# Optimization experiments

Measured on AMD Instinct MI355X. Metric: run time of the kernel, lower is better.

Reference implementation:

```python
import jax, jax.numpy as jnp
import numpy as np
import math

BATCH, TBINS, SPATIAL = 16, 8, 16
WIN, SHIFT = 8, 4
DIM, HEADS = 1024, 16
HD = DIM // HEADS
N = WIN * WIN          # tokens per window = 64
NW = (SPATIAL // WIN) ** 2  # windows per image = 4
HIDDEN = 4 * DIM


def _static_buffers():
    ws = WIN
    # continuous relative coords table (signed log-spaced), [(2ws-1)^2, 2]
    c = np.arange(-(ws - 1), ws, dtype=np.float32) / (ws - 1)
    c = np.sign(c) * np.log2(1.0 + np.abs(c))
    gh, gw = np.meshgrid(c, c, indexing='ij')
    table = np.stack([gh, gw], axis=-1).reshape(-1, 2).astype(np.float32)
    # relative position index, [N, N]
    coords = np.stack(np.meshgrid(np.arange(ws), np.arange(ws), indexing='ij')).reshape(2, -1)
    rel = (coords[:, :, None] - coords[:, None, :]).transpose(1, 2, 0)
    rel[..., 0] += ws - 1
    rel[..., 1] += ws - 1
    rel[..., 0] *= 2 * ws - 1
    rp_idx = rel.sum(-1)  # [N, N] int
    # shifted-window attention mask, [NW, N, N]
    img = np.zeros((SPATIAL, SPATIAL), dtype=np.float32)
    slices = [slice(0, -ws), slice(-ws, -SHIFT), slice(-SHIFT, None)]
    cnt = 0
    for hs in slices:
        for wsl in slices:
            img[hs, wsl] = cnt
            cnt += 1
    mw = img.reshape(SPATIAL // ws, ws, SPATIAL // ws, ws).transpose(0, 2, 1, 3).reshape(-1, ws * ws)
    diff = mw[:, None, :] - mw[:, :, None]  # matches unsqueeze(1) - unsqueeze(2)
    attn_mask = np.where(diff != 0, np.float32(-100.0), np.float32(0.0))
    return jnp.asarray(table), jnp.asarray(rp_idx), jnp.asarray(attn_mask)

CPB_TABLE, RP_IDX, ATTN_MASK = _static_buffers()


def _window_partition(x):  # [B, H, W, C] -> [B*nW, ws, ws, C]
    b, h, w, c = x.shape
    x = x.reshape(b, h // WIN, WIN, w // WIN, WIN, c).transpose(0, 1, 3, 2, 4, 5)
    return x.reshape(-1, WIN, WIN, c)


def _window_reverse(win, h, w):  # [B*nW, ws, ws, C] -> [B, H, W, C]
    b = win.shape[0] // ((h // WIN) * (w // WIN))
    x = win.reshape(b, h // WIN, w // WIN, WIN, WIN, -1).transpose(0, 1, 3, 2, 4, 5)
    return x.reshape(b, h, w, -1)


def _layernorm(x, g, b):
    m = jnp.mean(x, -1, keepdims=True)
    v = jnp.mean((x - m) ** 2, -1, keepdims=True)
    return (x - m) * jax.lax.rsqrt(v + 1e-5) * g + b


def _l2norm(x):
    return x / jnp.maximum(jnp.linalg.norm(x, axis=-1, keepdims=True), 1e-12)


def setup_inputs() -> dict:
    key = jax.random.key(0)
    ks = jax.random.split(key, 16)
    s = 0.02
    inp = {
        'x': jax.random.normal(ks[0], (BATCH, TBINS * SPATIAL * SPATIAL, DIM), jnp.float32),
        'qkv_w': jax.random.normal(ks[1], (3 * DIM, DIM), jnp.float32) * s,
        'q_bias': jnp.zeros((DIM,), jnp.float32),
        'v_bias': jnp.zeros((DIM,), jnp.float32),
        'logit_scale': jnp.full((HEADS, 1, 1), math.log(10.0), jnp.float32),
        'cpb_w1': jax.random.normal(ks[2], (512, 2), jnp.float32) * s,
        'cpb_b1': jnp.zeros((512,), jnp.float32),
        'cpb_w2': jax.random.normal(ks[3], (HEADS, 512), jnp.float32) * s,
        'proj_w': jax.random.normal(ks[4], (DIM, DIM), jnp.float32) * s,
        'proj_b': jnp.zeros((DIM,), jnp.float32),
        'norm1_w': jnp.ones((DIM,), jnp.float32),
        'norm1_b': jnp.zeros((DIM,), jnp.float32),
        'fc1_w': jax.random.normal(ks[5], (HIDDEN, DIM), jnp.float32) * s,
        'fc1_b': jnp.zeros((HIDDEN,), jnp.float32),
        'fc2_w': jax.random.normal(ks[6], (DIM, HIDDEN), jnp.float32) * s,
        'fc2_b': jnp.zeros((DIM,), jnp.float32),
        'norm2_w': jnp.ones((DIM,), jnp.float32),
        'norm2_b': jnp.zeros((DIM,), jnp.float32),
    }
    return inp


def reference(x, qkv_w, q_bias, v_bias, logit_scale, cpb_w1, cpb_b1, cpb_w2,
              proj_w, proj_b, norm1_w, norm1_b, fc1_w, fc1_b, fc2_w, fc2_b,
              norm2_w, norm2_b):
    B, L, C = x.shape
    xs = x.reshape(B * TBINS, SPATIAL, SPATIAL, C)
    shortcut = xs
    # cyclic shift
    shifted = jnp.roll(xs, shift=(-SHIFT, -SHIFT), axis=(1, 2))
    xw = _window_partition(shifted).reshape(-1, N, C)  # [Bw, N, C]
    Bw = xw.shape[0]

    # qkv with q/v bias only (no k bias)
    qkv_bias = jnp.concatenate([q_bias, jnp.zeros_like(v_bias), v_bias])
    qkv = xw @ qkv_w.T + qkv_bias
    qkv = qkv.reshape(Bw, N, 3, HEADS, HD).transpose(2, 0, 3, 1, 4)
    q, k, v = qkv[0], qkv[1], qkv[2]  # [Bw, h, N, hd]

    # cosine attention with clamped learnable logit scale
    attn = jnp.einsum('bhnd,bhmd->bhnm', _l2norm(q), _l2norm(k))
    scale = jnp.exp(jnp.minimum(logit_scale, math.log(100.0)))  # [h,1,1]
    attn = attn * scale[None]

    # continuous relative position bias via CPB-MLP
    tbl = jax.nn.relu(CPB_TABLE @ cpb_w1.T + cpb_b1) @ cpb_w2.T  # [(2ws-1)^2, h]
    tbl = 16.0 * jax.nn.sigmoid(tbl)
    bias = tbl[RP_IDX.reshape(-1)].reshape(N, N, HEADS).transpose(2, 0, 1)  # [h,N,N]
    attn = attn + bias[None]

    # shift mask
    attn = attn.reshape(Bw // NW, NW, HEADS, N, N) + ATTN_MASK[None, :, None]
    attn = attn.reshape(Bw, HEADS, N, N)
    attn = jax.nn.softmax(attn, axis=-1)

    out = jnp.einsum('bhnm,bhmd->bhnd', attn, v)
    out = out.transpose(0, 2, 1, 3).reshape(Bw, N, C)
    out = out @ proj_w.T + proj_b

    out = _window_reverse(out.reshape(-1, WIN, WIN, C), SPATIAL, SPATIAL)
    out = jnp.roll(out, shift=(SHIFT, SHIFT), axis=(1, 2))

    # SwinV2 post-norm residuals
    xs = shortcut + _layernorm(out, norm1_w, norm1_b)
    h = jax.nn.gelu(xs @ fc1_w.T + fc1_b, approximate=False) @ fc2_w.T + fc2_b
    xs = xs + _layernorm(h, norm2_w, norm2_b)
    return xs.reshape(B, L, C)
```

## Files before the change

kernel.cpp:

```cpp
#include <hip/hip_runtime.h>
#include <hip/hip_bf16.h>
#include <math.h>

typedef __hip_bfloat16 bf16;
typedef __attribute__((ext_vector_type(8))) short short8;
typedef __attribute__((ext_vector_type(4))) short short4v;
typedef __attribute__((ext_vector_type(4))) float floatx4;
typedef __attribute__((ext_vector_type(2))) unsigned int uint2v;

#define DEV static __device__ __forceinline__

DEV float bf2f(unsigned short u) {
  union { unsigned int i; float f; } x;
  x.i = ((unsigned int)u) << 16;
  return x.f;
}
DEV unsigned short f2bf_bits(float f) {
  union { bf16 h; unsigned short u; } x;
  x.h = __float2bfloat16(f);
  return x.u;
}
DEV short8 cvt8(float4 a, float4 b) {
  short8 r;
  r[0] = (short)f2bf_bits(a.x); r[1] = (short)f2bf_bits(a.y);
  r[2] = (short)f2bf_bits(a.z); r[3] = (short)f2bf_bits(a.w);
  r[4] = (short)f2bf_bits(b.x); r[5] = (short)f2bf_bits(b.y);
  r[6] = (short)f2bf_bits(b.z); r[7] = (short)f2bf_bits(b.w);
  return r;
}

DEV float gelu_fast(float v) {
  float y = v * (1.5957691216f + 0.0713548163f * v * v);
  return __fdividef(v, 1.f + __expf(-y));
}

DEV void gload_lds16(const unsigned short* g, unsigned short* l) {
  __builtin_amdgcn_global_load_lds((const __attribute__((address_space(1))) void*)g,
                                   (__attribute__((address_space(3))) void*)l,
                                   16, 0, 0);
}

DEV unsigned lds_addr(const void* p) {
  return (unsigned)(unsigned long long)(const __attribute__((address_space(3))) char*)p;
}

DEV int gather_win_row(int wr) {
  int bw = wr >> 6, n = wr & 63;
  int bt = bw >> 2, w2 = bw & 3;
  int wi = w2 >> 1, wj = w2 & 1;
  int r = n >> 3, c = n & 7;
  int sr = (wi * 8 + r + 4) & 15;
  int sc = (wj * 8 + c + 4) & 15;
  return bt * 256 + sr * 16 + sc;
}

enum { BIAS_SIMPLE = 0, BIAS_QKV = 1 };
enum { ACT_NONE = 0, ACT_GELU = 1 };

__global__ __launch_bounds__(256) void cvt_bf16(const float* __restrict__ in,
                                                bf16* __restrict__ out, int n) {
  int i = (blockIdx.x * 256 + threadIdx.x) * 8;
  if (i >= n) return;
  float4 a = *reinterpret_cast<const float4*>(in + i);
  float4 b = *reinterpret_cast<const float4*>(in + i + 4);
  *reinterpret_cast<short8*>((unsigned short*)out + i) = cvt8(a, b);
}

#define VMCNT(N_) asm volatile("s_waitcnt vmcnt(" #N_ ")" ::: "memory")
#define WAITLGKM() do { asm volatile("s_waitcnt lgkmcnt(0)" ::: "memory"); \
                        __builtin_amdgcn_sched_barrier(0); } while (0)
#define BARRIER() __builtin_amdgcn_s_barrier()
#define DSR(dst, addr, OFF) \
  asm volatile("ds_read_b128 %0, %1 offset:" #OFF : "=v"(dst) : "v"(addr) : "memory")

#define STG8(BUF, ISB, KS, KT) do { \
    unsigned short* d_ = (unsigned short*)(smem + (BUF) * 65536 + (ISB) * 32768 + (KS) * 16384); \
    gload_lds16(((ISB) ? bgp[0] : agp[0]) + (KT) * 64 + (KS) * 32, d_ + tid * 8); \
    gload_lds16(((ISB) ? bgp[1] : agp[1]) + (KT) * 64 + (KS) * 32, d_ + 4096 + tid * 8); \
  } while (0)

#define RD_A8(CUR, KS, IH) do { \
    unsigned a_ = smemBase + (CUR) * 65536 + (KS) * 16384 + aB0 + (IH) * 4096; \
    DSR(af[0], a_, 0); DSR(af[1], a_, 1024); DSR(af[2], a_, 2048); DSR(af[3], a_, 3072); \
  } while (0)

#define RD_B8(CUR, KS) do { \
    unsigned b_ = smemBase + (CUR) * 65536 + 32768 + (KS) * 16384 + bB0; \
    DSR(bfr[0], b_, 0); DSR(bfr[1], b_, 1024); DSR(bfr[2], b_, 2048); DSR(bfr[3], b_, 3072); \
  } while (0)

#define MFMA16(IH) do { \
    __builtin_amdgcn_s_setprio(1); \
    _Pragma("unroll") \
    for (int i_ = 0; i_ < 4; ++i_) \
      _Pragma("unroll") \
      for (int j_ = 0; j_ < 4; ++j_) \
        acc[(IH) * 4 + i_][j_] = __builtin_amdgcn_mfma_f32_16x16x32_bf16( \
            af[i_], bfr[j_], acc[(IH) * 4 + i_][j_], 0, 0, 0); \
    __builtin_amdgcn_s_setprio(0); \
  } while (0)

template <int GATHER, int BIASMODE, int ACT>
__global__ __launch_bounds__(512, 2) void gemm8p(
    const unsigned short* __restrict__ A, const unsigned short* __restrict__ B,
    const float* __restrict__ bias0, const float* __restrict__ bias1,
    bf16* __restrict__ C, int M, int N, int K)
{
  extern __shared__ __align__(16) char smem[];
  const int tid = threadIdx.x;
  const int lane = tid & 63;
  const int wave = tid >> 6;
  const int wm = wave >> 2, wn = wave & 3;
  const int l15 = lane & 15, g = lane >> 4;
  const int xr = (l15 >> 1) & 3;

  const int gy = gridDim.y;
  const int nwg = gridDim.x * gy;
  int lin = blockIdx.y * gridDim.x + blockIdx.x;
  if ((nwg & 7) == 0) lin = (lin & 7) * (nwg >> 3) + (lin >> 3);
  const int tileM = (lin / gy) * 256;
  const int tileN = (lin % gy) * 256;

  const unsigned short* agp[2];
  const unsigned short* bgp[2];
#pragma unroll
  for (int u = 0; u < 2; ++u) {
    int s = u * 512 + tid;
    int row = s >> 2;
    int dslot = (s & 3) ^ ((s >> 3) & 3);
    int gr = tileM + row;
    int sr = GATHER ? gather_win_row(gr) : gr;
    agp[u] = A + (size_t)sr * (size_t)K + dslot * 8;
    bgp[u] = B + (size_t)(tileN + row) * (size_t)K + dslot * 8;
  }

  const unsigned smemBase = lds_addr(smem);
  const unsigned aB0 = (unsigned)((wm * 128 + l15) * 64 + ((g ^ xr) * 16));
  const unsigned bB0 = (unsigned)((wn * 64 + l15) * 64 + ((g ^ xr) * 16));

  floatx4 acc[8][4];
#pragma unroll
  for (int i = 0; i < 8; ++i)
#pragma unroll
    for (int j = 0; j < 4; ++j) acc[i][j] = (floatx4){0.f, 0.f, 0.f, 0.f};

  short8 af[4], bfr[4];
  const int NT = K >> 6;
  int cur = 0;

  STG8(0, 0, 0, 0); STG8(0, 1, 0, 0); STG8(0, 0, 1, 0); STG8(0, 1, 1, 0);
  VMCNT(0);
  BARRIER();

  for (int t = 0; t < NT - 1; ++t) {
    const int nb = cur ^ 1;
    RD_B8(cur, 0); RD_A8(cur, 0, 0);
    STG8(nb, 0, 0, t + 1);
    BARRIER(); WAITLGKM(); MFMA16(0); BARRIER();
    RD_A8(cur, 0, 1);
    STG8(nb, 1, 0, t + 1);
    VMCNT(4);
    BARRIER(); WAITLGKM(); MFMA16(1); BARRIER();
    RD_B8(cur, 1); RD_A8(cur, 1, 0);
    STG8(nb, 0, 1, t + 1);
    BARRIER(); WAITLGKM(); MFMA16(0); BARRIER();
    RD_A8(cur, 1, 1);
    STG8(nb, 1, 1, t + 1);
    VMCNT(4);
    BARRIER(); WAITLGKM(); MFMA16(1); BARRIER();
    cur = nb;
  }
  RD_B8(cur, 0); RD_A8(cur, 0, 0);
  BARRIER(); WAITLGKM(); MFMA16(0); BARRIER();
  RD_A8(cur, 0, 1);
  VMCNT(0);
  BARRIER(); WAITLGKM(); MFMA16(1); BARRIER();
  RD_B8(cur, 1); RD_A8(cur, 1, 0);
  BARRIER(); WAITLGKM(); MFMA16(0); BARRIER();
  RD_A8(cur, 1, 1);
  WAITLGKM(); MFMA16(1);

  __syncthreads();
  unsigned short* sh16 = (unsigned short*)smem;
  const int q = l15;
  float bv[4];
#pragma unroll
  for (int j = 0; j < 4; ++j) {
    const int colG = tileN + wn * 64 + j * 16 + q;
    if (BIASMODE == BIAS_QKV) {
      bv[j] = (colG < 1024) ? bias0[colG] : (colG < 2048 ? 0.f : bias1[colG - 2048]);
    } else {
      bv[j] = bias0[colG];
    }
  }
#pragma unroll
  for (int h = 0; h < 2; ++h) {
    if (wm == h) {
#pragma unroll
      for (int i = 0; i < 8; ++i)
#pragma unroll
        for (int j = 0; j < 4; ++j)
#pragma unroll
          for (int r = 0; r < 4; ++r) {
            float v = acc[i][j][r] + bv[j];
            if (ACT == ACT_GELU) v = gelu_fast(v);
            sh16[(i * 16 + g * 4 + r) * 264 + wn * 64 + j * 16 + q] = f2bf_bits(v);
          }
    }
    __syncthreads();
#pragma unroll
    for (int pass = 0; pass < 8; ++pass) {
      const int idx = pass * 512 + tid;
      const int row = idx >> 5, c16 = idx & 31;
      uint4 val = *reinterpret_cast<const uint4*>(&sh16[row * 264 + c16 * 8]);
      *reinterpret_cast<uint4*>(
          (unsigned short*)C + (size_t)(tileM + h * 128 + row) * (size_t)N +
          tileN + c16 * 8) = val;
    }
    __syncthreads();
  }
}

#define STG_A2(BUF, KS, KT) do { \
    unsigned short* d_ = (unsigned short*)(smem + (BUF) * 49152 + (KS) * 16384); \
    gload_lds16(agp[0] + (KT) * 64 + (KS) * 32, d_ + tid * 8); \
    gload_lds16(agp[1] + (KT) * 64 + (KS) * 32, d_ + 4096 + tid * 8); \
  } while (0)

#define STG_B1(BUF, KS, KT) do { \
    unsigned short* d_ = (unsigned short*)(smem + (BUF) * 49152 + 32768 + (KS) * 8192); \
    gload_lds16(bgp0 + (KT) * 64 + (KS) * 32, d_ + tid * 8); \
  } while (0)

#define RD_A8N(CUR, KS, IH) do { \
    unsigned a_ = smemBase + (CUR) * 49152 + (KS) * 16384 + aB0 + (IH) * 4096; \
    DSR(af[0], a_, 0); DSR(af[1], a_, 1024); DSR(af[2], a_, 2048); DSR(af[3], a_, 3072); \
  } while (0)

#define RD_B2N(CUR, KS) do { \
    unsigned b_ = smemBase + (CUR) * 49152 + 32768 + (KS) * 8192 + bB0; \
    DSR(bfr[0], b_, 0); DSR(bfr[1], b_, 1024); \
  } while (0)

#define MFMA8(IH) do { \
    __builtin_amdgcn_s_setprio(1); \
    _Pragma("unroll") \
    for (int i_ = 0; i_ < 4; ++i_) \
      _Pragma("unroll") \
      for (int j_ = 0; j_ < 2; ++j_) \
        acc[(IH) * 4 + i_][j_] = __builtin_amdgcn_mfma_f32_16x16x32_bf16( \
            af[i_], bfr[j_], acc[(IH) * 4 + i_][j_], 0, 0, 0); \
    __builtin_amdgcn_s_setprio(0); \
  } while (0)

template <int GATHER, int BIASMODE, int ACT>
__global__ __launch_bounds__(512, 2) void gemm8pn(
    const unsigned short* __restrict__ A, const unsigned short* __restrict__ B,
    const float* __restrict__ bias0, const float* __restrict__ bias1,
    bf16* __restrict__ C, int M, int N, int K)
{
  extern __shared__ __align__(16) char smem[];
  const int tid = threadIdx.x;
  const int lane = tid & 63;
  const int wave = tid >> 6;
  const int wm = wave >> 2, wn = wave & 3;
  const int l15 = lane & 15, g = lane >> 4;
  const int xr = (l15 >> 1) & 3;

  const int gy = gridDim.y;
  const int nwg = gridDim.x * gy;
  int lin = blockIdx.y * gridDim.x + blockIdx.x;
  if ((nwg & 7) == 0) lin = (lin & 7) * (nwg >> 3) + (lin >> 3);
  const int tileM = (lin / gy) * 256;
  const int tileN = (lin % gy) * 128;

  const unsigned short* agp[2];
#pragma unroll
  for (int u = 0; u < 2; ++u) {
    int s = u * 512 + tid;
    int row = s >> 2;
    int dslot = (s & 3) ^ ((s >> 3) & 3);
    int gr = tileM + row;
    int sr = GATHER ? gather_win_row(gr) : gr;
    agp[u] = A + (size_t)sr * (size_t)K + dslot * 8;
  }
  const unsigned short* bgp0 =
      B + (size_t)(tileN + (tid >> 2)) * (size_t)K + ((tid & 3) ^ ((tid >> 3) & 3)) * 8;

  const unsigned smemBase = lds_addr(smem);
  const unsigned aB0 = (unsigned)((wm * 128 + l15) * 64 + ((g ^ xr) * 16));
  const unsigned bB0 = (unsigned)((wn * 32 + l15) * 64 + ((g ^ xr) * 16));

  floatx4 acc[8][2];
#pragma unroll
  for (int i = 0; i < 8; ++i)
#pragma unroll
    for (int j = 0; j < 2; ++j) acc[i][j] = (floatx4){0.f, 0.f, 0.f, 0.f};

  short8 af[4], bfr[2];
  const int NT = K >> 6;
  int cur = 0;

  STG_A2(0, 0, 0); STG_B1(0, 0, 0); STG_A2(0, 1, 0); STG_B1(0, 1, 0);
  VMCNT(0);
  BARRIER();

  for (int t = 0; t < NT - 1; ++t) {
    const int nb = cur ^ 1;
    RD_B2N(cur, 0); RD_A8N(cur, 0, 0);
    STG_A2(nb, 0, t + 1);
    BARRIER(); WAITLGKM(); MFMA8(0); BARRIER();
    RD_A8N(cur, 0, 1);
    STG_B1(nb, 0, t + 1);
    VMCNT(3);
    BARRIER(); WAITLGKM(); MFMA8(1); BARRIER();
    RD_B2N(cur, 1); RD_A8N(cur, 1, 0);
    STG_A2(nb, 1, t + 1);
    BARRIER(); WAITLGKM(); MFMA8(0); BARRIER();
    RD_A8N(cur, 1, 1);
    STG_B1(nb, 1, t + 1);
    VMCNT(3);
    BARRIER(); WAITLGKM(); MFMA8(1); BARRIER();
    cur = nb;
  }
  RD_B2N(cur, 0); RD_A8N(cur, 0, 0);
  BARRIER(); WAITLGKM(); MFMA8(0); BARRIER();
  RD_A8N(cur, 0, 1);
  VMCNT(0);
  BARRIER(); WAITLGKM(); MFMA8(1); BARRIER();
  RD_B2N(cur, 1); RD_A8N(cur, 1, 0);
  BARRIER(); WAITLGKM(); MFMA8(0); BARRIER();
  RD_A8N(cur, 1, 1);
  WAITLGKM(); MFMA8(1);

  __syncthreads();
  unsigned short* sh16 = (unsigned short*)smem;
  const int q = l15;
  float bv[2];
#pragma unroll
  for (int j = 0; j < 2; ++j) {
    const int colG = tileN + wn * 32 + j * 16 + q;
    if (BIASMODE == BIAS_QKV) {
      bv[j] = (colG < 1024) ? bias0[colG] : (colG < 2048 ? 0.f : bias1[colG - 2048]);
    } else {
      bv[j] = bias0[colG];
    }
  }
#pragma unroll
  for (int h = 0; h < 2; ++h) {
    if (wm == h) {
#pragma unroll
      for (int i = 0; i < 8; ++i)
#pragma unroll
        for (int j = 0; j < 2; ++j)
#pragma unroll
          for (int r = 0; r < 4; ++r) {
            float v = acc[i][j][r] + bv[j];
            if (ACT == ACT_GELU) v = gelu_fast(v);
            sh16[(i * 16 + g * 4 + r) * 136 + wn * 32 + j * 16 + q] = f2bf_bits(v);
          }
    }
    __syncthreads();
#pragma unroll
    for (int pass = 0; pass < 4; ++pass) {
      const int idx = pass * 512 + tid;
      const int row = idx >> 4, c16 = idx & 15;
      uint4 val = *reinterpret_cast<const uint4*>(&sh16[row * 136 + c16 * 8]);
      *reinterpret_cast<uint4*>(
          (unsigned short*)C + (size_t)(tileM + h * 128 + row) * (size_t)N +
          tileN + c16 * 8) = val;
    }
    __syncthreads();
  }
}

template <int GATHER, int BIASMODE, int ACT>
__global__ __launch_bounds__(256, 2) void gemm_bt(
    const unsigned short* __restrict__ A, const unsigned short* __restrict__ B,
    const float* __restrict__ bias0, const float* __restrict__ bias1,
    bf16* __restrict__ C, int M, int N, int K)
{
  __shared__ __align__(16) unsigned short sh[128 * 136];
  unsigned short* As = sh;
  unsigned short* Bs = sh + 8192;

  const int tid = threadIdx.x;
  const int lane = tid & 63;
  const int wave = tid >> 6;
  const int waveM = wave >> 1, waveN = wave & 1;
  const int tileM = blockIdx.x * 128, tileN = blockIdx.y * 128;

  const int row0 = tid >> 3;
  const int kOff = (tid & 7) * 8;

  const unsigned short* ag[4];
  const unsigned short* bg[4];
  unsigned short* al[4];
  unsigned short* bl[4];
#pragma unroll
  for (int t = 0; t < 4; ++t) {
    int gr = tileM + row0 + 32 * t;
    int sr = GATHER ? gather_win_row(gr) : gr;
    ag[t] = A + (size_t)sr * (size_t)K + (size_t)kOff;
    bg[t] = B + (size_t)(tileN + row0 + 32 * t) * (size_t)K + (size_t)kOff;
    al[t] = &As[(row0 + 32 * t) * 64 + kOff];
    bl[t] = &Bs[(row0 + 32 * t) * 64 + kOff];
  }

  floatx4 acc[4][4];
#pragma unroll
  for (int i = 0; i < 4; ++i)
#pragma unroll
    for (int j = 0; j < 4; ++j) acc[i][j] = (floatx4){0.f, 0.f, 0.f, 0.f};

  for (int k0 = 0; k0 < K; k0 += 64) {
#pragma unroll
    for (int t = 0; t < 4; ++t) {
      gload_lds16(ag[t] + k0, al[t]);
      gload_lds16(bg[t] + k0, bl[t]);
    }
    __syncthreads();
#pragma unroll
    for (int ks = 0; ks < 2; ++ks) {
      const int kk = ks * 32 + (lane >> 4) * 8;
      short8 afv[4], bfv[4];
#pragma unroll
      for (int i = 0; i < 4; ++i)
        afv[i] = *reinterpret_cast<const short8*>(
            &As[(waveM * 64 + i * 16 + (lane & 15)) * 64 + kk]);
#pragma unroll
      for (int j = 0; j < 4; ++j)
        bfv[j] = *reinterpret_cast<const short8*>(
            &Bs[(waveN * 64 + j * 16 + (lane & 15)) * 64 + kk]);
#pragma unroll
      for (int i = 0; i < 4; ++i)
#pragma unroll
        for (int j = 0; j < 4; ++j)
          acc[i][j] = __builtin_amdgcn_mfma_f32_16x16x32_bf16(afv[i], bfv[j], acc[i][j], 0, 0, 0);
    }
    __syncthreads();
  }

#pragma unroll
  for (int j = 0; j < 4; ++j) {
    const int colL = waveN * 64 + j * 16 + (lane & 15);
    const int colG = tileN + colL;
    float bv;
    if (BIASMODE == BIAS_QKV) {
      if (colG < 1024) bv = bias0[colG];
      else if (colG < 2048) bv = 0.f;
      else bv = bias1[colG - 2048];
    } else {
      bv = bias0[colG];
    }
#pragma unroll
    for (int i = 0; i < 4; ++i) {
      const int rL = waveM * 64 + i * 16 + ((lane >> 4) * 4);
#pragma unroll
      for (int r = 0; r < 4; ++r) {
        float v = acc[i][j][r] + bv;
        if (ACT == ACT_GELU) v = gelu_fast(v);
        sh[(rL + r) * 136 + colL] = f2bf_bits(v);
      }
    }
  }
  __syncthreads();
  {
    const int rowR = tid >> 4;
    const int colR = (tid & 15) * 8;
#pragma unroll
    for (int s = 0; s < 8; ++s) {
      const int row = s * 16 + rowR;
      uint4 val = *reinterpret_cast<const uint4*>(&sh[row * 136 + colR]);
      *reinterpret_cast<uint4*>(
          (unsigned short*)C + (size_t)(tileM + row) * (size_t)N + tileN + colR) = val;
    }
  }
}

__global__ __launch_bounds__(512) void cpb_kernel(
    const float* __restrict__ w1, const float* __restrict__ b1,
    const float* __restrict__ w2, float* __restrict__ TBL)
{
  __shared__ float hid[512];
  const int i = blockIdx.x;
  const int j = threadIdx.x;
  const float d0 = ((float)(i / 15) - 7.f) / 7.f;
  const float d1 = ((float)(i % 15) - 7.f) / 7.f;
  const float t0 = copysignf(log2f(1.f + fabsf(d0)), d0);
  const float t1 = copysignf(log2f(1.f + fabsf(d1)), d1);
  float hv = t0 * w1[j * 2] + t1 * w1[j * 2 + 1] + b1[j];
  hid[j] = fmaxf(hv, 0.f);
  __syncthreads();
  if (j < 16) {
    float s = 0.f;
    for (int jj = 0; jj < 512; ++jj) s += w2[j * 512 + jj] * hid[jj];
    TBL[j * 225 + i] = 16.f / (1.f + expf(-s));
  }
}

__global__ __launch_bounds__(256) void attn_mfma(
    const bf16* __restrict__ QKV, const float* __restrict__ TBL,
    const float* __restrict__ ls, bf16* __restrict__ ATT)
{
  __shared__ __align__(16) unsigned short Ps[4][64][72];
  __shared__ float tbs[4][226];
  __shared__ int ids[64];

  const int tid = threadIdx.x;
  const int w = tid >> 6;
  const int l = tid & 63;
  const int q = l & 15;
  const int g = l >> 4;
  const int bw = blockIdx.x >> 2;
  const int h = (blockIdx.x & 3) * 4 + w;

  const unsigned short* qkvu = (const unsigned short*)QKV;
  const size_t rbase = (size_t)(bw * 64) * 3072;

  if (tid < 64) {
    const int w2 = bw & 3, wi = w2 >> 1, wj = w2 & 1;
    const int r = tid >> 3, c = tid & 7;
    const int rr = (wi == 0) ? 0 : (r < 4 ? 1 : 2);
    const int rc = (wj == 0) ? 0 : (c < 4 ? 1 : 2);
    ids[tid] = rr * 3 + rc;
  }
#pragma unroll
  for (int i = 0; i < 4; ++i) {
    int idx = i * 64 + l;
    if (idx < 225) tbs[w][idx] = TBL[h * 225 + idx];
  }
  __syncthreads();

  short8 kf[4][2], qf[4][2];
#pragma unroll
  for (int i = 0; i < 4; ++i) {
    const unsigned short* rp = qkvu + rbase + (size_t)(16 * i + q) * 3072 + h * 64 + g * 8;
    qf[i][0] = *reinterpret_cast<const short8*>(rp);
    qf[i][1] = *reinterpret_cast<const short8*>(rp + 32);
    kf[i][0] = *reinterpret_cast<const short8*>(rp + 1024);
    kf[i][1] = *reinterpret_cast<const short8*>(rp + 1024 + 32);
  }

  float rk4[4], rq4[4];
#pragma unroll
  for (int i = 0; i < 4; ++i) {
    float sk = 0.f, sq = 0.f;
#pragma unroll
    for (int ks = 0; ks < 2; ++ks)
#pragma unroll
      for (int e = 0; e < 8; ++e) {
        float kv = bf2f((unsigned short)kf[i][ks][e]);
        float qv = bf2f((unsigned short)qf[i][ks][e]);
        sk += kv * kv; sq += qv * qv;
      }
    sk += __shfl_xor(sk, 16); sk += __shfl_xor(sk, 32);
    sq += __shfl_xor(sq, 16); sq += __shfl_xor(sq, 32);
    rk4[i] = 1.f / fmaxf(sqrtf(sk), 1e-12f);
    rq4[i] = 1.f / fmaxf(sqrtf(sq), 1e-12f);
  }
  const float scl = expf(fminf(ls[h], 4.60517019f));
  float rqs[4];
#pragma unroll
  for (int j = 0; j < 4; ++j) rqs[j] = rq4[j] * scl;

  floatx4 acc[4][4];
#pragma unroll
  for (int i = 0; i < 4; ++i)
#pragma unroll
    for (int j = 0; j < 4; ++j) acc[i][j] = (floatx4){0.f, 0.f, 0.f, 0.f};
#pragma unroll
  for (int ks = 0; ks < 2; ++ks)
#pragma unroll
    for (int i = 0; i < 4; ++i)
#pragma unroll
      for (int j = 0; j < 4; ++j)
        acc[i][j] = __builtin_amdgcn_mfma_f32_16x16x32_bf16(kf[i][ks], qf[j][ks], acc[i][j], 0, 0, 0);

  short8 vf[4][2];
  const unsigned short* vbase = qkvu + rbase + 2048 + h * 64;
#pragma unroll
  for (int jp = 0; jp < 4; ++jp)
#pragma unroll
    for (int ks = 0; ks < 2; ++ks) {
      const int m0 = ks * 32 + g * 8;
      const unsigned short* vp = vbase + 16 * jp + q;
      union { short8 v; unsigned short u[8]; } pk;
#pragma unroll
      for (int e = 0; e < 8; ++e)
        pk.u[e] = vp[(size_t)(m0 + e) * 3072];
      vf[jp][ks] = pk.v;
    }

  int idn[4], rtn[4], ctn[4];
#pragma unroll
  for (int j = 0; j < 4; ++j) {
    const int n = 16 * j + q;
    rtn[j] = n >> 3; ctn[j] = n & 7; idn[j] = ids[n];
  }
#pragma unroll
  for (int i = 0; i < 4; ++i) {
#pragma unroll
    for (int r = 0; r < 4; ++r) {
      const int m = 16 * i + 4 * g + r;
      const float rkm = __shfl(rk4[i], 4 * g + r);
      const int rm = m >> 3, cm = m & 7;
      const int idm = ids[m];
#pragma unroll
      for (int j = 0; j < 4; ++j) {
        float v = acc[i][j][r] * (rkm * rqs[j]) +
                  tbs[w][(rtn[j] - rm + 7) * 15 + (ctn[j] - cm + 7)];
        if (idm != idn[j]) v -= 100.f;
        acc[i][j][r] = v;
      }
    }
  }

  float rs4[4];
#pragma unroll
  for (int j = 0; j < 4; ++j) {
    float mx = acc[0][j][0];
#pragma unroll
    for (int i = 0; i < 4; ++i)
#pragma unroll
      for (int r = 0; r < 4; ++r) mx = fmaxf(mx, acc[i][j][r]);
    mx = fmaxf(mx, __shfl_xor(mx, 16));
    mx = fmaxf(mx, __shfl_xor(mx, 32));
    float sm = 0.f;
#pragma unroll
    for (int i = 0; i < 4; ++i)
#pragma unroll
      for (int r = 0; r < 4; ++r) {
        float e = __expf(acc[i][j][r] - mx);
        acc[i][j][r] = e; sm += e;
      }
    sm += __shfl_xor(sm, 16);
    sm += __shfl_xor(sm, 32);
    rs4[j] = 1.f / sm;
  }

#pragma unroll
  for (int j = 0; j < 4; ++j)
#pragma unroll
    for (int i = 0; i < 4; ++i) {
      uint2v pw;
      pw[0] = (unsigned int)f2bf_bits(acc[i][j][0]) |
              ((unsigned int)f2bf_bits(acc[i][j][1]) << 16);
      pw[1] = (unsigned int)f2bf_bits(acc[i][j][2]) |
              ((unsigned int)f2bf_bits(acc[i][j][3]) << 16);
      *reinterpret_cast<uint2v*>(&Ps[w][16 * j + q][16 * i + 4 * g]) = pw;
    }

  floatx4 o[4][4];
#pragma unroll
  for (int i = 0; i < 4; ++i)
#pragma unroll
    for (int j = 0; j < 4; ++j) o[i][j] = (floatx4){0.f, 0.f, 0.f, 0.f};
#pragma unroll
  for (int ks = 0; ks < 2; ++ks) {
    short8 pa[4];
#pragma unroll
    for (int i2 = 0; i2 < 4; ++i2)
      pa[i2] = *reinterpret_cast<const short8*>(&Ps[w][16 * i2 + q][ks * 32 + g * 8]);
#pragma unroll
    for (int i2 = 0; i2 < 4; ++i2)
#pragma unroll
      for (int j2 = 0; j2 < 4; ++j2)
        o[i2][j2] = __builtin_amdgcn_mfma_f32_16x16x32_bf16(pa[i2], vf[j2][ks], o[i2][j2], 0, 0, 0);
  }

  unsigned short* op = (unsigned short*)ATT + (size_t)(bw * 64) * 1024 + h * 64;
#pragma unroll
  for (int i2 = 0; i2 < 4; ++i2)
#pragma unroll
    for (int r = 0; r < 4; ++r) {
      const float rsn = __shfl(rs4[i2], 4 * g + r);
      const int row = 16 * i2 + 4 * g + r;
#pragma unroll
      for (int j2 = 0; j2 < 4; ++j2)
        op[(size_t)row * 1024 + 16 * j2 + q] = f2bf_bits(o[i2][j2][r] * rsn);
    }
}

template <bool GATHER, bool WB>
__global__ __launch_bounds__(256) void ln_residual(
    const bf16* __restrict__ src, const float* base,
    const float* __restrict__ gw, const float* __restrict__ gb,
    float* out, bf16* __restrict__ out_bf)
{
  const int tok = blockIdx.x * 4 + (threadIdx.x >> 6);
  const int lane = threadIdx.x & 63;
  int srow;
  if (GATHER) {
    const int bt = tok >> 8, rem = tok & 255, i = rem >> 4, j = rem & 15;
    const int p = (i + 12) & 15, qq = (j + 12) & 15;
    srow = (bt * 4 + (p >> 3) * 2 + (qq >> 3)) * 64 + (p & 7) * 8 + (qq & 7);
  } else {
    srow = tok;
  }
  const unsigned short* sp = (const unsigned short*)src + (size_t)srow * 1024 + lane * 16;
  short8 lv0 = *reinterpret_cast<const short8*>(sp);
  short8 lv1 = *reinterpret_cast<const short8*>(sp + 8);
  float v[16];
  float s = 0.f, sq = 0.f;
#pragma unroll
  for (int u = 0; u < 8; ++u) {
    float f = bf2f((unsigned short)lv0[u]); v[u] = f; s += f; sq += f * f;
    float g = bf2f((unsigned short)lv1[u]); v[u + 8] = g; s += g; sq += g * g;
  }
#pragma unroll
  for (int off = 32; off > 0; off >>= 1) { s += __shfl_xor(s, off); sq += __shfl_xor(sq, off); }
  const float mean = s * (1.f / 1024.f);
  const float var = sq * (1.f / 1024.f) - mean * mean;
  const float rstd = rsqrtf(var + 1e-5f);

  const float* bp = base + (size_t)tok * 1024 + lane * 16;
  float* op = out + (size_t)tok * 1024 + lane * 16;
  unsigned short* obp = WB ? ((unsigned short*)out_bf + (size_t)tok * 1024 + lane * 16) : nullptr;
  union { short8 v; unsigned short u[8]; } ob0, ob1;
#pragma unroll
  for (int q4 = 0; q4 < 4; ++q4) {
    float4 b4 = *reinterpret_cast<const float4*>(bp + q4 * 4);
    float bl[4] = {b4.x, b4.y, b4.z, b4.w};
    float4 o4;
    float* ol = (float*)&o4;
#pragma unroll
    for (int u = 0; u < 4; ++u) {
      const int c = lane * 16 + q4 * 4 + u;
      ol[u] = bl[u] + (v[q4 * 4 + u] - mean) * rstd * gw[c] + gb[c];
      if (WB) {
        if (q4 < 2) ob0.u[q4 * 4 + u] = f2bf_bits(ol[u]);
        else ob1.u[(q4 - 2) * 4 + u] = f2bf_bits(ol[u]);
      }
    }
    *reinterpret_cast<float4*>(op + q4 * 4) = o4;
  }
  if (WB) {
    *reinterpret_cast<short8*>(obp) = ob0.v;
    *reinterpret_cast<short8*>(obp + 8) = ob1.v;
  }
}

extern "C" void kernel_launch(void* const* d_in, const int* in_sizes, int n_in,
                              void* d_out, int out_size, void* d_ws, size_t ws_size,
                              hipStream_t stream) {
  (void)in_sizes; (void)n_in; (void)out_size;
  const float* x      = (const float*)d_in[0];
  const float* qkv_w  = (const float*)d_in[1];
  const float* q_bias = (const float*)d_in[2];
  const float* v_bias = (const float*)d_in[3];
  const float* lscale = (const float*)d_in[4];
  const float* cpb_w1 = (const float*)d_in[5];
  const float* cpb_b1 = (const float*)d_in[6];
  const float* cpb_w2 = (const float*)d_in[7];
  const float* proj_w = (const float*)d_in[8];
  const float* proj_b = (const float*)d_in[9];
  const float* n1w    = (const float*)d_in[10];
  const float* n1b    = (const float*)d_in[11];
  const float* fc1_w  = (const float*)d_in[12];
  const float* fc1_b  = (const float*)d_in[13];
  const float* fc2_w  = (const float*)d_in[14];
  const float* fc2_b  = (const float*)d_in[15];
  const float* n2w    = (const float*)d_in[16];
  const float* n2b    = (const float*)d_in[17];
  float* out = (float*)d_out;

  static int attr_ok = -1;
  if (attr_ok < 0) {
    hipError_t e1 = hipFuncSetAttribute(
        reinterpret_cast<const void*>(&gemm8p<0, BIAS_SIMPLE, ACT_GELU>),
        hipFuncAttributeMaxDynamicSharedMemorySize, 131072);
    hipError_t e2 = hipFuncSetAttribute(
        reinterpret_cast<const void*>(&gemm8pn<1, BIAS_QKV, ACT_NONE>),
        hipFuncAttributeMaxDynamicSharedMemorySize, 98304);
    hipError_t e3 = hipFuncSetAttribute(
        reinterpret_cast<const void*>(&gemm8pn<0, BIAS_SIMPLE, ACT_NONE>),
        hipFuncAttributeMaxDynamicSharedMemorySize, 98304);
    attr_ok = (e1 == hipSuccess && e2 == hipSuccess && e3 == hipSuccess) ? 1 : 0;
  }

  char* ws = (char*)d_ws;
  bf16*  QKV  = (bf16*)(ws);
  bf16*  H    = (bf16*)(ws);
  bf16*  ATT  = (bf16*)(ws + 67108864);
  bf16*  XSB  = (bf16*)(ws + 67108864);
  bf16*  F2   = (bf16*)(ws + 67108864);
  bf16*  XBF  = (bf16*)(ws + 83886080);
  bf16*  PROJ = (bf16*)(ws + 83886080);
  float* TBL  = (float*)(ws + 100663296);

  const bool persist = ws_size >= (size_t)125845504;
  bf16* WQKV, *WPROJ, *WF1, *WF2;
  if (persist) {
    WQKV  = (bf16*)(ws + 100679680);
    WPROJ = (bf16*)(ws + 106971136);
    WF1   = (bf16*)(ws + 109068288);
    WF2   = (bf16*)(ws + 117456896);
  } else {
    WQKV  = (bf16*)(ws + 67108864);
    WPROJ = (bf16*)(ws + 50331648);
    WF1   = (bf16*)(ws + 83886080);
    WF2   = (bf16*)(ws + 83886080 + 8388608);
  }

  cpb_kernel<<<225, 512, 0, stream>>>(cpb_w1, cpb_b1, cpb_w2, TBL);
  if (persist) {
    cvt_bf16<<<1536, 256, 0, stream>>>(qkv_w, WQKV, 3145728);
    cvt_bf16<<<512, 256, 0, stream>>>(proj_w, WPROJ, 1048576);
    cvt_bf16<<<2048, 256, 0, stream>>>(fc1_w, WF1, 4194304);
    cvt_bf16<<<2048, 256, 0, stream>>>(fc2_w, WF2, 4194304);
  }

  for (int ch = 0; ch < 4; ++ch) {
    const size_t tokBase = (size_t)ch * 8192;
    const float* x_c = x + tokBase * 1024;
    float* out_c = out + tokBase * 1024;

    cvt_bf16<<<4096, 256, 0, stream>>>(x_c, XBF, 8388608);
    if (!persist) {
      cvt_bf16<<<1536, 256, 0, stream>>>(qkv_w, WQKV, 3145728);
      cvt_bf16<<<512, 256, 0, stream>>>(proj_w, WPROJ, 1048576);
    }

    if (attr_ok) {
      gemm8pn<1, BIAS_QKV, ACT_NONE><<<dim3(32, 24), 512, 98304, stream>>>(
          (const unsigned short*)XBF, (const unsigned short*)WQKV,
          q_bias, v_bias, QKV, 8192, 3072, 1024);
    } else {
      gemm_bt<1, BIAS_QKV, ACT_NONE><<<dim3(64, 24), 256, 0, stream>>>(
          (const unsigned short*)XBF, (const unsigned short*)WQKV,
          q_bias, v_bias, QKV, 8192, 3072, 1024);
    }
    attn_mfma<<<512, 256, 0, stream>>>(QKV, TBL, lscale, ATT);
    if (attr_ok) {
      gemm8pn<0, BIAS_SIMPLE, ACT_NONE><<<dim3(32, 8), 512, 98304, stream>>>(
          (const unsigned short*)ATT, (const unsigned short*)WPROJ,
          proj_b, nullptr, PROJ, 8192, 1024, 1024);
    } else {
      gemm_bt<0, BIAS_SIMPLE, ACT_NONE><<<dim3(64, 8), 256, 0, stream>>>(
          (const unsigned short*)ATT, (const unsigned short*)WPROJ,
          proj_b, nullptr, PROJ, 8192, 1024, 1024);
    }
    ln_residual<true, true><<<2048, 256, 0, stream>>>(PROJ, x_c, n1w, n1b, out_c, XSB);
    if (!persist) {
      cvt_bf16<<<2048, 256, 0, stream>>>(fc1_w, WF1, 4194304);
      cvt_bf16<<<2048, 256, 0, stream>>>(fc2_w, WF2, 4194304);
    }
    if (attr_ok) {
      gemm8p<0, BIAS_SIMPLE, ACT_GELU><<<dim3(32, 16), 512, 131072, stream>>>(
          (const unsigned short*)XSB, (const unsigned short*)WF1,
          fc1_b, nullptr, H, 8192, 4096, 1024);
      gemm8pn<0, BIAS_SIMPLE, ACT_NONE><<<dim3(32, 8), 512, 98304, stream>>>(
          (const unsigned short*)H, (const unsigned short*)WF2,
          fc2_b, nullptr, F2, 8192, 1024, 4096);
    } else {
      gemm_bt<0, BIAS_SIMPLE, ACT_GELU><<<dim3(64, 32), 256, 0, stream>>>(
          (const unsigned short*)XSB, (const unsigned short*)WF1,
          fc1_b, nullptr, H, 8192, 4096, 1024);
      gemm_bt<0, BIAS_SIMPLE, ACT_NONE><<<dim3(64, 8), 256, 0, stream>>>(
          (const unsigned short*)H, (const unsigned short*)WF2,
          fc2_b, nullptr, F2, 8192, 1024, 4096);
    }
    ln_residual<false, false><<<2048, 256, 0, stream>>>(F2, out_c, n2w, n2b, out_c, nullptr);
  }
}
```

Baseline: 1.575 ms.

## Double-buffer LDS fragment registers to overlap ds_reads with MFMA in GEMM kernels

Both GEMM kernels now keep two register sets for A and B fragments and issue the LDS reads for the next sub-step before running the MFMAs on the current one. Partial lgkmcnt waits replace the full waits, so the loads are hidden behind matrix compute, and the first fragments of the next k-tile are prefetched at the end of each iteration. The cost is more VGPRs, which may threaten the two-blocks-per-CU occupancy target. The barrier ordering around buffer reuse also becomes harder to reason about.

```diff
diff --git a/kernel.cpp b/kernel.cpp
--- a/kernel.cpp
+++ b/kernel.cpp
@@ -67,8 +67,8 @@
 }
 
 #define VMCNT(N_) asm volatile("s_waitcnt vmcnt(" #N_ ")" ::: "memory")
-#define WAITLGKM() do { asm volatile("s_waitcnt lgkmcnt(0)" ::: "memory"); \
-                        __builtin_amdgcn_sched_barrier(0); } while (0)
+#define LGKM(N_) do { asm volatile("s_waitcnt lgkmcnt(" #N_ ")" ::: "memory"); \
+                      __builtin_amdgcn_sched_barrier(0); } while (0)
 #define BARRIER() __builtin_amdgcn_s_barrier()
 #define DSR(dst, addr, OFF) \
   asm volatile("ds_read_b128 %0, %1 offset:" #OFF : "=v"(dst) : "v"(addr) : "memory")
@@ -79,24 +79,26 @@
     gload_lds16(((ISB) ? bgp[1] : agp[1]) + (KT) * 64 + (KS) * 32, d_ + 4096 + tid * 8); \
   } while (0)
 
-#define RD_A8(CUR, KS, IH) do { \
+#define RD_A8S(ST, CUR, KS, IH) do { \
     unsigned a_ = smemBase + (CUR) * 65536 + (KS) * 16384 + aB0 + (IH) * 4096; \
-    DSR(af[0], a_, 0); DSR(af[1], a_, 1024); DSR(af[2], a_, 2048); DSR(af[3], a_, 3072); \
+    DSR(af[ST][0], a_, 0); DSR(af[ST][1], a_, 1024); \
+    DSR(af[ST][2], a_, 2048); DSR(af[ST][3], a_, 3072); \
   } while (0)
 
-#define RD_B8(CUR, KS) do { \
+#define RD_B8S(ST, CUR, KS) do { \
     unsigned b_ = smemBase + (CUR) * 65536 + 32768 + (KS) * 16384 + bB0; \
-    DSR(bfr[0], b_, 0); DSR(bfr[1], b_, 1024); DSR(bfr[2], b_, 2048); DSR(bfr[3], b_, 3072); \
+    DSR(bfr[ST][0], b_, 0); DSR(bfr[ST][1], b_, 1024); \
+    DSR(bfr[ST][2], b_, 2048); DSR(bfr[ST][3], b_, 3072); \
   } while (0)
 
-#define MFMA16(IH) do { \
+#define MFMA16S(IH, AS, BS) do { \
     __builtin_amdgcn_s_setprio(1); \
     _Pragma("unroll") \
     for (int i_ = 0; i_ < 4; ++i_) \
       _Pragma("unroll") \
       for (int j_ = 0; j_ < 4; ++j_) \
         acc[(IH) * 4 + i_][j_] = __builtin_amdgcn_mfma_f32_16x16x32_bf16( \
-            af[i_], bfr[j_], acc[(IH) * 4 + i_][j_], 0, 0, 0); \
+            af[AS][i_], bfr[BS][j_], acc[(IH) * 4 + i_][j_], 0, 0, 0); \
     __builtin_amdgcn_s_setprio(0); \
   } while (0)
 
@@ -144,41 +146,51 @@
 #pragma unroll
     for (int j = 0; j < 4; ++j) acc[i][j] = (floatx4){0.f, 0.f, 0.f, 0.f};
 
-  short8 af[4], bfr[4];
+  short8 af[2][4], bfr[2][4];
   const int NT = K >> 6;
   int cur = 0;
 
   STG8(0, 0, 0, 0); STG8(0, 1, 0, 0); STG8(0, 0, 1, 0); STG8(0, 1, 1, 0);
   VMCNT(0);
   BARRIER();
+  RD_B8S(0, 0, 0); RD_A8S(0, 0, 0, 0);
 
   for (int t = 0; t < NT - 1; ++t) {
     const int nb = cur ^ 1;
-    RD_B8(cur, 0); RD_A8(cur, 0, 0);
     STG8(nb, 0, 0, t + 1);
-    BARRIER(); WAITLGKM(); MFMA16(0); BARRIER();
-    RD_A8(cur, 0, 1);
+    BARRIER();
+    RD_A8S(1, cur, 0, 1);
+    LGKM(4); MFMA16S(0, 0, 0);
+    BARRIER();
     STG8(nb, 1, 0, t + 1);
     VMCNT(4);
-    BARRIER(); WAITLGKM(); MFMA16(1); BARRIER();
-    RD_B8(cur, 1); RD_A8(cur, 1, 0);
+    BARRIER();
+    RD_B8S(1, cur, 1); RD_A8S(0, cur, 1, 0);
+    LGKM(8); MFMA16S(1, 1, 0);
+    BARRIER();
     STG8(nb, 0, 1, t + 1);
-    BARRIER(); WAITLGKM(); MFMA16(0); BARRIER();
-    RD_A8(cur, 1, 1);
+    BARRIER();
+    RD_A8S(1, cur, 1, 1);
+    LGKM(4); MFMA16S(0, 0, 1);
+    BARRIER();
     STG8(nb, 1, 1, t + 1);
     VMCNT(4);
-    BARRIER(); WAITLGKM(); MFMA16(1); BARRIER();
+    BARRIER();
+    RD_B8S(0, nb, 0); RD_A8S(0, nb, 0, 0);
+    LGKM(8); MFMA16S(1, 1, 1);
+    BARRIER();
     cur = nb;
   }
-  RD_B8(cur, 0); RD_A8(cur, 0, 0);
-  BARRIER(); WAITLGKM(); MFMA16(0); BARRIER();
-  RD_A8(cur, 0, 1);
+  RD_A8S(1, cur, 0, 1);
+  LGKM(4); MFMA16S(0, 0, 0);
+  BARRIER();
   VMCNT(0);
-  BARRIER(); WAITLGKM(); MFMA16(1); BARRIER();
-  RD_B8(cur, 1); RD_A8(cur, 1, 0);
-  BARRIER(); WAITLGKM(); MFMA16(0); BARRIER();
-  RD_A8(cur, 1, 1);
-  WAITLGKM(); MFMA16(1);
+  BARRIER();
+  RD_B8S(1, cur, 1); RD_A8S(0, cur, 1, 0);
+  LGKM(8); MFMA16S(1, 1, 0);
+  RD_A8S(1, cur, 1, 1);
+  LGKM(4); MFMA16S(0, 0, 1);
+  LGKM(0); MFMA16S(1, 1, 1);
 
   __syncthreads();
   unsigned short* sh16 = (unsigned short*)smem;
@@ -232,24 +244,25 @@
     gload_lds16(bgp0 + (KT) * 64 + (KS) * 32, d_ + tid * 8); \
   } while (0)
 
-#define RD_A8N(CUR, KS, IH) do { \
+#define RD_A8NS(ST, CUR, KS, IH) do { \
     unsigned a_ = smemBase + (CUR) * 49152 + (KS) * 16384 + aB0 + (IH) * 4096; \
-    DSR(af[0], a_, 0); DSR(af[1], a_, 1024); DSR(af[2], a_, 2048); DSR(af[3], a_, 3072); \
+    DSR(af[ST][0], a_, 0); DSR(af[ST][1], a_, 1024); \
+    DSR(af[ST][2], a_, 2048); DSR(af[ST][3], a_, 3072); \
   } while (0)
 
-#define RD_B2N(CUR, KS) do { \
+#define RD_B2NS(ST, CUR, KS) do { \
     unsigned b_ = smemBase + (CUR) * 49152 + 32768 + (KS) * 8192 + bB0; \
-    DSR(bfr[0], b_, 0); DSR(bfr[1], b_, 1024); \
+    DSR(bfr[ST][0], b_, 0); DSR(bfr[ST][1], b_, 1024); \
   } while (0)
 
-#define MFMA8(IH) do { \
+#define MFMA8S(IH, AS, BS) do { \
     __builtin_amdgcn_s_setprio(1); \
     _Pragma("unroll") \
     for (int i_ = 0; i_ < 4; ++i_) \
       _Pragma("unroll") \
       for (int j_ = 0; j_ < 2; ++j_) \
         acc[(IH) * 4 + i_][j_] = __builtin_amdgcn_mfma_f32_16x16x32_bf16( \
-            af[i_], bfr[j_], acc[(IH) * 4 + i_][j_], 0, 0, 0); \
+            af[AS][i_], bfr[BS][j_], acc[(IH) * 4 + i_][j_], 0, 0, 0); \
     __builtin_amdgcn_s_setprio(0); \
   } while (0)
 
@@ -297,41 +310,51 @@
 #pragma unroll
     for (int j = 0; j < 2; ++j) acc[i][j] = (floatx4){0.f, 0.f, 0.f, 0.f};
 
-  short8 af[4], bfr[2];
+  short8 af[2][4], bfr[2][2];
   const int NT = K >> 6;
   int cur = 0;
 
   STG_A2(0, 0, 0); STG_B1(0, 0, 0); STG_A2(0, 1, 0); STG_B1(0, 1, 0);
   VMCNT(0);
   BARRIER();
+  RD_B2NS(0, 0, 0); RD_A8NS(0, 0, 0, 0);
 
   for (int t = 0; t < NT - 1; ++t) {
     const int nb = cur ^ 1;
-    RD_B2N(cur, 0); RD_A8N(cur, 0, 0);
     STG_A2(nb, 0, t + 1);
-    BARRIER(); WAITLGKM(); MFMA8(0); BARRIER();
-    RD_A8N(cur, 0, 1);
+    BARRIER();
+    RD_A8NS(1, cur, 0, 1);
+    LGKM(4); MFMA8S(0, 0, 0);
+    BARRIER();
     STG_B1(nb, 0, t + 1);
     VMCNT(3);
-    BARRIER(); WAITLGKM(); MFMA8(1); BARRIER();
-    RD_B2N(cur, 1); RD_A8N(cur, 1, 0);
+    BARRIER();
+    RD_B2NS(1, cur, 1); RD_A8NS(0, cur, 1, 0);
+    LGKM(6); MFMA8S(1, 1, 0);
+    BARRIER();
     STG_A2(nb, 1, t + 1);
-    BARRIER(); WAITLGKM(); MFMA8(0); BARRIER();
-    RD_A8N(cur, 1, 1);
+    BARRIER();
+    RD_A8NS(1, cur, 1, 1);
+    LGKM(4); MFMA8S(0, 0, 1);
+    BARRIER();
     STG_B1(nb, 1, t + 1);
     VMCNT(3);
-    BARRIER(); WAITLGKM(); MFMA8(1); BARRIER();
+    BARRIER();
+    RD_B2NS(0, nb, 0); RD_A8NS(0, nb, 0, 0);
+    LGKM(6); MFMA8S(1, 1, 1);
+    BARRIER();
     cur = nb;
   }
-  RD_B2N(cur, 0); RD_A8N(cur, 0, 0);
-  BARRIER(); WAITLGKM(); MFMA8(0); BARRIER();
-  RD_A8N(cur, 0, 1);
+  RD_A8NS(1, cur, 0, 1);
+  LGKM(4); MFMA8S(0, 0, 0);
+  BARRIER();
   VMCNT(0);
-  BARRIER(); WAITLGKM(); MFMA8(1); BARRIER();
-  RD_B2N(cur, 1); RD_A8N(cur, 1, 0);
-  BARRIER(); WAITLGKM(); MFMA8(0); BARRIER();
-  RD_A8N(cur, 1, 1);
-  WAITLGKM(); MFMA8(1);
+  BARRIER();
+  RD_B2NS(1, cur, 1); RD_A8NS(0, cur, 1, 0);
+  LGKM(6); MFMA8S(1, 1, 0);
+  RD_A8NS(1, cur, 1, 1);
+  LGKM(4); MFMA8S(0, 0, 1);
+  LGKM(0); MFMA8S(1, 1, 1);
 
   __syncthreads();
   unsigned short* sh16 = (unsigned short*)smem;
```

After: 1.574 ms. Within noise of the previous version (-0.1%).
